# Kernel tuning notes

Measured on AMD Instinct MI355X. Metric: run time of the kernel, lower is better.

## Reference

```python
import jax, jax.numpy as jnp
import numpy as np

D = 128; H = 8; L = 3; FF = 512; HID = 512
B = 512; N = 20
KD = D // H
CLIP = 10.0


def _bn(x, g, b):
    # BatchNorm1d over flattened (B*n, D), training-mode batch stats, affine
    m = jnp.mean(x, axis=(0, 1)); v = jnp.var(x, axis=(0, 1))
    return (x - m) * jax.lax.rsqrt(v + 1e-5) * g + b


def _mha(x, Wq, Wk, Wv, Wo):
    q = jnp.einsum('bnd,hdk->hbnk', x, Wq)
    k = jnp.einsum('bnd,hdk->hbnk', x, Wk)
    v = jnp.einsum('bnd,hdk->hbnk', x, Wv)
    a = jax.nn.softmax(jnp.einsum('hbnk,hbmk->hbnm', q, k) / np.float32(np.sqrt(KD)), axis=-1)
    h = jnp.einsum('hbnm,hbmk->hbnk', a, v)
    return jnp.einsum('hbnk,hkd->bnd', h, Wo)


def _encode(x, Wq, Wk, Wv, Wo, g1, b1, fW1, fb1, fW2, fb2, g2, b2):
    for l in range(L):
        x = _bn(x + _mha(x, Wq[l], Wk[l], Wv[l], Wo[l]), g1[l], b1[l])
        f = jnp.maximum(x @ fW1[l] + fb1[l], 0.0) @ fW2[l] + fb2[l]
        x = _bn(x + f, g2[l], b2[l])
    return x


def _forward(coords, Wi, bi, W_ph, enc_Wq, enc_Wk, enc_Wv, enc_Wo, enc_g1, enc_b1,
             enc_ffW1, enc_ffb1, enc_ffW2, enc_ffb2, enc_g2, enc_b2,
             W_node, W_fixed, W_step, W_out, Wc1, bc1, Wc2, bc2):
    Bs, Ns, _ = coords.shape
    bid = jnp.arange(Bs)
    x = coords @ Wi + bi                                   # (B,N,D) initial embeddings
    crd = coords
    node_idx = jnp.broadcast_to(jnp.arange(Ns)[None, :], (Bs, Ns))
    # state is re-made each step, so step context is always the placeholder
    step_ctx = jnp.broadcast_to(W_ph[None, :], (Bs, 2 * D))
    ctx_q = step_ctx @ W_step                              # (B,D), constant across steps
    log_ps = []; irs = []; vals = []; tours = []
    first = prev = cur = None
    for i in range(Ns):  # sequential decode loop (shapes shrink each step)
        n = Ns - i
        E = _encode(x, enc_Wq, enc_Wk, enc_Wv, enc_Wo, enc_g1, enc_b1,
                    enc_ffW1, enc_ffb1, enc_ffW2, enc_ffb2, enc_g2, enc_b2)  # (B,n,D)
        g_mean = jnp.mean(E, axis=1)                       # (B,D)
        q = g_mean @ W_fixed + ctx_q                       # (B,D)
        gK, gV, lK = jnp.split(E @ W_node, 3, axis=-1)     # each (B,n,D)
        qh = q.reshape(Bs, H, KD)
        a = jax.nn.softmax(jnp.einsum('bhk,bnhk->bhn', qh, gK.reshape(Bs, n, H, KD)) / np.float32(np.sqrt(KD)), axis=-1)
        glimpse = jnp.einsum('bhn,bnhk->bhk', a, gV.reshape(Bs, n, H, KD)).reshape(Bs, D) @ W_out
        logits = jnp.tanh(jnp.einsum('bd,bnd->bn', glimpse, lK) / np.float32(np.sqrt(D))) * CLIP
        log_p = jax.nn.log_softmax(logits, axis=-1)        # mask all-False (fresh state)
        sel = jnp.argmax(log_p, axis=1)                    # greedy decode
        log_ps.append(log_p[bid, sel])
        cur = crd[bid, sel]
        if i == 0:
            first = cur
            irs.append(jnp.zeros((Bs,), coords.dtype))
        else:
            irs.append(-jnp.sqrt(jnp.sum((cur - prev) ** 2, axis=1)))
        h = jnp.maximum(jnp.concatenate([g_mean, step_ctx], axis=1) @ Wc1 + bc1, 0.0)
        vals.append((h @ Wc2 + bc2)[:, 0])
        tours.append(node_idx[bid, sel])
        if i < Ns - 1:
            sel_mask = (jnp.arange(n)[None, :] == sel[:, None]).astype(jnp.int32)
            keep = jnp.argsort(sel_mask, axis=1)[:, : n - 1]  # stable: drops selected, keeps order
            crd = jnp.take_along_axis(crd, keep[:, :, None], axis=1)
            x = jnp.take_along_axis(x, keep[:, :, None], axis=1)
            node_idx = jnp.take_along_axis(node_idx, keep, axis=1)
        prev = cur
    reward_final = -jnp.sqrt(jnp.sum((first - cur) ** 2, axis=1))
    tours = jnp.stack(tours, axis=1)                        # (B,N) int
    d = jnp.take_along_axis(coords, tours[:, :, None], axis=1)
    cost = jnp.sum(jnp.linalg.norm(d[:, 1:] - d[:, :-1], axis=2), axis=1) + jnp.linalg.norm(d[:, 0] - d[:, -1], axis=1)
    return (jnp.stack(log_ps, 1), jnp.stack(irs, 1), jnp.stack(vals, 1), cost, reward_final, tours)


def setup_inputs():
    key = jax.random.key(0)
    ks = jax.random.split(key, 16)
    def nrm(k, shp, scale=0.02):
        return jax.random.normal(k, shp, dtype=jnp.float32) * scale
    return {
        'coords': jax.random.uniform(ks[0], (B, N, 2), dtype=jnp.float32),
        'Wi': nrm(ks[1], (2, D), 0.5),
        'bi': jnp.zeros((D,), jnp.float32),
        'W_ph': jax.random.uniform(ks[2], (2 * D,), jnp.float32, -1.0, 1.0),
        'enc_Wq': nrm(ks[3], (L, H, D, KD)),
        'enc_Wk': nrm(ks[4], (L, H, D, KD)),
        'enc_Wv': nrm(ks[5], (L, H, D, KD)),
        'enc_Wo': nrm(ks[6], (L, H, KD, D)),
        'enc_g1': jnp.ones((L, D), jnp.float32),
        'enc_b1': jnp.zeros((L, D), jnp.float32),
        'enc_ffW1': nrm(ks[7], (L, D, FF)),
        'enc_ffb1': jnp.zeros((L, FF), jnp.float32),
        'enc_ffW2': nrm(ks[8], (L, FF, D)),
        'enc_ffb2': jnp.zeros((L, D), jnp.float32),
        'enc_g2': jnp.ones((L, D), jnp.float32),
        'enc_b2': jnp.zeros((L, D), jnp.float32),
        'W_node': nrm(ks[9], (D, 3 * D)),
        'W_fixed': nrm(ks[10], (D, D)),
        'W_step': nrm(ks[11], (2 * D, D)),
        'W_out': nrm(ks[12], (D, D)),
        'Wc1': nrm(ks[13], (3 * D, HID)),
        'bc1': jnp.zeros((HID,), jnp.float32),
        'Wc2': nrm(ks[14], (HID, 1)),
        'bc2': jnp.zeros((1,), jnp.float32),
    }


def reference(coords, Wi, bi, W_ph, enc_Wq, enc_Wk, enc_Wv, enc_Wo, enc_g1, enc_b1,
              enc_ffW1, enc_ffb1, enc_ffW2, enc_ffb2, enc_g2, enc_b2,
              W_node, W_fixed, W_step, W_out, Wc1, bc1, Wc2, bc2):
    return _forward(coords, Wi, bi, W_ph, enc_Wq, enc_Wk, enc_Wv, enc_Wo, enc_g1, enc_b1,
                    enc_ffW1, enc_ffb1, enc_ffW2, enc_ffb2, enc_g2, enc_b2,
                    W_node, W_fixed, W_step, W_out, Wc1, bc1, Wc2, bc2)
```

## Files before the change

### kernel.cpp

```cpp
#include <hip/hip_runtime.h>
#include <cmath>

namespace {
constexpr int Hc = 8, FFc = 512, HIDc = 512;
}

struct Params {
  const float *coords, *Wi, *bi, *W_ph;
  const float *Wq, *Wk, *Wv, *Wo, *g1, *b1, *fW1, *fb1, *fW2, *fb2, *g2, *b2;
  const float *W_node, *W_fixed, *W_step, *W_out, *Wc1, *bc1, *Wc2, *bc2;
  float* out;
};

__device__ __align__(16) float g_bn[120 * 8 * 256];
__device__ __align__(16) float g_x[512 * 2560];
__device__ __align__(16) float g_t[512 * 2560];
__device__ __align__(16) float g_h[512 * 2560];
__device__ __align__(16) float g_dec[512 * 7680];
__device__ __align__(16) float g_qv[512 * 128];
__device__ float g_val[512];
__device__ __align__(16) float g_crd[512 * 40];
__device__ int   g_idx[512 * 20];
__device__ float g_state[512 * 8];
__device__ __align__(16) float g_ctxq[128];
__device__ __align__(16) float g_cctx[512];
__device__ __align__(16) float g_Wqp[3 * 16384];
__device__ __align__(16) float g_Wkp[3 * 16384];
__device__ __align__(16) float g_Wvp[3 * 16384];
__device__ __align__(16) float g_Wop[3 * 16384];
__device__ __align__(16) float g_W1q[3 * 65536];
__device__ __align__(16) float g_W2q[3 * 65536];
__device__ __align__(16) float g_Wnp[49152];
__device__ __align__(16) float g_Wfp[16384];
__device__ __align__(16) float g_Woup[16384];
__device__ __align__(16) float g_Wc1p[65536];

#define DOT4(a, b) ((a).x*(b).x + (a).y*(b).y + (a).z*(b).z + (a).w*(b).w)

__device__ __forceinline__ void bn_coef(int slot, const float* g, const float* bb, float cnt,
                                        float* s_scale, float* s_shift, int tid) {
  if (tid < 128) {
    float sm = 0.f, sq = 0.f;
#pragma unroll
    for (int r = 0; r < 8; r++) {
      const float* s = &g_bn[(slot * 8 + r) * 256];
      sm += s[tid]; sq += s[128 + tid];
    }
    float m_ = sm / cnt;
    float v_ = sq / cnt - m_ * m_;
    float rs = rsqrtf(v_ + 1e-5f);
    float sc = rs * g[tid];
    s_scale[tid] = sc;
    s_shift[tid] = bb[tid] - m_ * sc;
  }
}

__global__ __launch_bounds__(256) void kinit(Params p) {
  const int tid = threadIdx.x, b = blockIdx.x;
  const int gid = b * 256 + tid, GS = 512 * 256;
  for (int i = gid; i < 120 * 8 * 256; i += GS) g_bn[i] = 0.f;
  if (gid < 512) g_val[gid] = 0.f;
  for (int e = tid; e < 2560; e += 256) {
    int i = e >> 7, d = e & 127;
    float cx = p.coords[b * 40 + 2 * i], cy = p.coords[b * 40 + 2 * i + 1];
    g_x[b * 2560 + e] = cx * p.Wi[d] + cy * p.Wi[128 + d] + p.bi[d];
  }
  if (tid < 40) g_crd[b * 40 + tid] = p.coords[b * 40 + tid];
  if (tid < 20) g_idx[b * 20 + tid] = tid;
  if (tid < 8) g_state[b * 8 + tid] = 0.f;
  if (b == 0) {
    if (tid < 128) {
      float a = 0.f;
      for (int j = 0; j < 256; j++) a += p.W_ph[j] * p.W_step[j * 128 + tid];
      g_ctxq[tid] = a;
    }
    for (int jj = tid; jj < 512; jj += 256) {
      float a = p.bc1[jj];
      for (int e = 0; e < 256; e++) a += p.W_ph[e] * p.Wc1[(128 + e) * 512 + jj];
      g_cctx[jj] = a;
    }
  }
  for (int e = gid; e < 3 * 16384; e += GS) {
    int sub = e & 3, rest = e >> 2;
    int j = rest & 127, rest2 = rest >> 7, d4 = rest2 & 31, l = rest2 >> 5;
    int d = d4 * 4 + sub;
    int src = l * 16384 + (j >> 4) * 2048 + d * 16 + (j & 15);
    g_Wqp[e] = p.Wq[src]; g_Wkp[e] = p.Wk[src]; g_Wvp[e] = p.Wv[src];
    int c = d;
    g_Wop[e] = p.Wo[l * 16384 + (c >> 4) * 2048 + (c & 15) * 128 + j];
  }
  for (int e = gid; e < 3 * 65536; e += GS) {
    int sub = e & 3, f = (e >> 2) & 16383, l = e >> 16;
    int cg = f & 127, c = (f >> 7) & 3, k4 = f >> 9;
    g_W1q[e] = p.fW1[l * 65536 + (k4 * 4 + sub) * 512 + cg * 4 + c];
  }
  for (int e = gid; e < 3 * 65536; e += GS) {
    int sub = e & 3, f = (e >> 2) & 16383, l = e >> 16;
    int j = f & 127, k4 = f >> 7;
    g_W2q[e] = p.fW2[l * 65536 + (k4 * 4 + sub) * 128 + j];
  }
  for (int e = gid; e < 49152; e += GS) {
    int sub = e & 3, rest = e >> 2;
    int col = rest % 384, e4 = rest / 384;
    g_Wnp[e] = p.W_node[(e4 * 4 + sub) * 384 + col];
  }
  for (int e = gid; e < 16384; e += GS) {
    int sub = e & 3, rest = e >> 2;
    int j = rest & 127, e4 = rest >> 7;
    g_Wfp[e] = p.W_fixed[(e4 * 4 + sub) * 128 + j];
    g_Woup[e] = p.W_out[(e4 * 4 + sub) * 128 + j];
  }
  for (int e = gid; e < 65536; e += GS) {
    int sub = e & 3, rest = e >> 2;
    int jj = rest & 511, e4 = rest >> 9;
    g_Wc1p[e] = p.Wc1[(e4 * 4 + sub) * 512 + jj];
  }
}

__global__ __launch_bounds__(256, 4) void ka1(Params p, int step, int l) {
  const int tid = threadIdx.x, b = blockIdx.x, hb = blockIdx.y;
  const int n = 20 - step;
  const int jc = tid & 63, rg = tid >> 6;
  __shared__ __align__(16) float s_t[2560];
  __shared__ __align__(16) float s_q[1280];
  __shared__ float s_kT[1280];
  __shared__ __align__(16) float s_v[1280];
  __shared__ float s_att[1600];
  __shared__ __align__(16) float s_scale[128], s_shift[128];

  if (l > 0)
    bn_coef(step * 6 + (l - 1) * 2 + 1, p.g2 + (l - 1) * 128, p.b2 + (l - 1) * 128,
            (float)(512 * n), s_scale, s_shift, tid);
  __syncthreads();
  const float4* src4 = (const float4*)((l == 0 ? g_x : g_t) + b * 2560);
  float4* st4 = (float4*)s_t;
  for (int e4 = tid; e4 < n * 32; e4 += 256) {
    float4 x = src4[e4];
    if (l > 0) {
      float4 sc = ((const float4*)s_scale)[e4 & 31];
      float4 sh = ((const float4*)s_shift)[e4 & 31];
      x.x = x.x * sc.x + sh.x; x.y = x.y * sc.y + sh.y;
      x.z = x.z * sc.z + sh.z; x.w = x.w * sc.w + sh.w;
    }
    st4[e4] = x;
  }
  __syncthreads();
  {
    const int j = hb * 64 + jc;
    const float4* wq4 = (const float4*)g_Wqp + l * 4096 + j;
    const float4* wk4 = (const float4*)g_Wkp + l * 4096 + j;
    const float4* wv4 = (const float4*)g_Wvp + l * 4096 + j;
    float aq[5], ak[5], av[5];
#pragma unroll
    for (int r = 0; r < 5; r++) { aq[r] = 0.f; ak[r] = 0.f; av[r] = 0.f; }
    float4 bq = wq4[0], bk = wk4[0], bv = wv4[0];
#pragma unroll 2
    for (int d4 = 0; d4 < 32; d4++) {
      const int dn = (d4 + 1) & 31;
      float4 nq = wq4[dn * 128], nk = wk4[dn * 128], nv = wv4[dn * 128];
#pragma unroll
      for (int r = 0; r < 5; r++) {
        int i = rg + 4 * r;
        if (i < n) {
          float4 x = st4[i * 32 + d4];
          aq[r] += DOT4(x, bq); ak[r] += DOT4(x, bk); av[r] += DOT4(x, bv);
        }
      }
      bq = nq; bk = nk; bv = nv;
    }
#pragma unroll
    for (int r = 0; r < 5; r++) {
      int i = rg + 4 * r;
      if (i < n) {
        s_q[i * 64 + jc] = aq[r];
        s_kT[jc * 20 + i] = ak[r];
        s_v[i * 64 + jc] = av[r];
      }
    }
  }
  __syncthreads();
  const int nn = n * n;
  for (int e = tid; e < 4 * nn; e += 256) {
    int hl = e / nn, rem = e % nn, i = rem / n, m = rem % n;
    float dacc = 0.f;
#pragma unroll
    for (int k2 = 0; k2 < 16; k2++)
      dacc += s_q[i * 64 + hl * 16 + k2] * s_kT[(hl * 16 + k2) * 20 + m];
    s_att[hl * 400 + i * 20 + m] = dacc * 0.25f;
  }
  __syncthreads();
  for (int r = tid; r < 4 * n; r += 256) {
    int hl = r / n, i = r % n;
    float* row = s_att + hl * 400 + i * 20;
    float mx = row[0];
    for (int m = 1; m < n; m++) mx = fmaxf(mx, row[m]);
    float s = 0.f;
    for (int m = 0; m < n; m++) { float ev = __expf(row[m] - mx); row[m] = ev; s += ev; }
    float inv = 1.f / s;
    for (int m = 0; m < n; m++) row[m] *= inv;
  }
  __syncthreads();
  for (int e = tid; e < 4 * n * 16; e += 256) {
    int hl = e / (n * 16), rem = e % (n * 16), i = rem >> 4, k2 = rem & 15;
    const float* arow = s_att + hl * 400 + i * 20;
    float acc = 0.f;
    for (int m = 0; m < n; m++) acc += arow[m] * s_v[m * 64 + hl * 16 + k2];
    g_h[b * 2560 + i * 128 + hb * 64 + hl * 16 + k2] = acc;
  }
}

__global__ __launch_bounds__(256, 4) void ka2(Params p, int step, int l) {
  const int tid = threadIdx.x, b = blockIdx.x, s = blockIdx.y;
  const int n = 20 - step;
  const int jcol = tid & 127, rhalf = tid >> 7;
  __shared__ __align__(16) float s_h[2560];
  __shared__ __align__(16) float s_x[2560];
  __shared__ __align__(16) float s_scale[128], s_shift[128];
  __shared__ float s_sm[128], s_sq[128];

  if (l > 0)
    bn_coef(step * 6 + (l - 1) * 2 + 1, p.g2 + (l - 1) * 128, p.b2 + (l - 1) * 128,
            (float)(512 * n), s_scale, s_shift, tid);
  __syncthreads();
  const float4* src4 = (const float4*)((l == 0 ? g_x : g_t) + b * 2560);
  const float4* gh4 = (const float4*)(g_h + b * 2560);
  float4* sh4 = (float4*)s_h;
  float4* sx4 = (float4*)s_x;
  for (int e4 = tid; e4 < n * 32; e4 += 256) {
    int i = e4 >> 5;
    if (((i ^ s) & 1) == 0) {
      sh4[e4] = gh4[e4];
      float4 x = src4[e4];
      if (l > 0) {
        float4 sc = ((const float4*)s_scale)[e4 & 31];
        float4 sf = ((const float4*)s_shift)[e4 & 31];
        x.x = x.x * sc.x + sf.x; x.y = x.y * sc.y + sf.y;
        x.z = x.z * sc.z + sf.z; x.w = x.w * sc.w + sf.w;
      }
      sx4[e4] = x;
    }
  }
  __syncthreads();
  float acc[5];
#pragma unroll
  for (int r = 0; r < 5; r++) {
    int i = s + 2 * (rhalf + 2 * r);
    acc[r] = (i < n) ? s_x[i * 128 + jcol] : 0.f;
  }
  const float4* wo4 = (const float4*)g_Wop + l * 4096 + jcol;
  float4 wb0 = wo4[0], wb1 = wo4[128];
#pragma unroll 2
  for (int c4 = 0; c4 < 32; c4++) {
    float4 wn = wo4[((c4 + 2) & 31) * 128];
#pragma unroll
    for (int r = 0; r < 5; r++) {
      int i = s + 2 * (rhalf + 2 * r);
      if (i < n) { float4 h = sh4[i * 32 + c4]; acc[r] += DOT4(h, wb0); }
    }
    wb0 = wb1; wb1 = wn;
  }
  float sm = 0.f, sq = 0.f;
#pragma unroll
  for (int r = 0; r < 5; r++) {
    int i = s + 2 * (rhalf + 2 * r);
    if (i < n) { g_t[b * 2560 + i * 128 + jcol] = acc[r]; sm += acc[r]; sq += acc[r] * acc[r]; }
  }
  __syncthreads();
  if (rhalf == 1) { s_sm[jcol] = sm; s_sq[jcol] = sq; }
  __syncthreads();
  if (rhalf == 0) {
    float* slot = &g_bn[((step * 6 + l * 2) * 8 + ((b * 2 + s) & 7)) * 256];
    atomicAdd(&slot[jcol], sm + s_sm[jcol]);
    atomicAdd(&slot[128 + jcol], sq + s_sq[jcol]);
  }
}

__global__ __launch_bounds__(256, 4) void kff(Params p, int step, int l) {
  const int tid = threadIdx.x, bx = blockIdx.x;
  const int n = 20 - step;
  const int r0 = bx * 16;
  const int wid = tid >> 6, lam = tid & 63;
  const int g = wid >> 1, rh = wid & 1;
  __shared__ __align__(16) float s_x[16 * 128];
  __shared__ __align__(16) float s_hid[16 * 512];
  __shared__ __align__(16) float s_scale[128], s_shift[128];
  __shared__ float s_bn[8 * 128 * 2];

  bn_coef(step * 6 + l * 2, p.g1 + l * 128, p.b1 + l * 128, (float)(512 * n), s_scale, s_shift, tid);
  __syncthreads();
  {
    float4* sx4 = (float4*)s_x;
    for (int e4 = tid; e4 < 16 * 32; e4 += 256) {
      int row = e4 >> 5, d4 = e4 & 31;
      int r = r0 + row, b = r / n, i = r - b * n;
      float4 x = *(const float4*)(g_t + b * 2560 + i * 128 + d4 * 4);
      float4 sc = ((const float4*)s_scale)[d4];
      float4 sf = ((const float4*)s_shift)[d4];
      x.x = x.x * sc.x + sf.x; x.y = x.y * sc.y + sf.y;
      x.z = x.z * sc.z + sf.z; x.w = x.w * sc.w + sf.w;
      sx4[e4] = x;
    }
  }
  __syncthreads();
  {
    const int cg = g * 64 + lam;
    float acc[8][4];
#pragma unroll
    for (int rr = 0; rr < 8; rr++)
#pragma unroll
      for (int c = 0; c < 4; c++) acc[rr][c] = 0.f;
    const float4* w1 = (const float4*)g_W1q + l * 16384 + cg;
    const float4* xx = (const float4*)s_x + rh * 8 * 32;
    float4 wb[4];
#pragma unroll
    for (int c = 0; c < 4; c++) wb[c] = w1[c * 128];
#pragma unroll 2
    for (int k4 = 0; k4 < 32; k4++) {
      float4 wn[4];
      const int kn = (k4 + 1) & 31;
#pragma unroll
      for (int c = 0; c < 4; c++) wn[c] = w1[kn * 512 + c * 128];
#pragma unroll
      for (int rr = 0; rr < 8; rr++) {
        float4 xr = xx[rr * 32 + k4];
#pragma unroll
        for (int c = 0; c < 4; c++) acc[rr][c] += DOT4(xr, wb[c]);
      }
#pragma unroll
      for (int c = 0; c < 4; c++) wb[c] = wn[c];
    }
    float4 b1v = *(const float4*)(p.fb1 + l * FFc + cg * 4);
#pragma unroll
    for (int rr = 0; rr < 8; rr++) {
      int row = rh * 8 + rr;
      float4 u;
      u.x = fmaxf(acc[rr][0] + b1v.x, 0.f); u.y = fmaxf(acc[rr][1] + b1v.y, 0.f);
      u.z = fmaxf(acc[rr][2] + b1v.z, 0.f); u.w = fmaxf(acc[rr][3] + b1v.w, 0.f);
      *(float4*)&s_hid[row * 512 + cg * 4] = u;
    }
  }
  __syncthreads();
  {
    const int j = g * 64 + lam;
    float acc[8];
#pragma unroll
    for (int rr = 0; rr < 8; rr++) acc[rr] = 0.f;
    const float4* w2 = (const float4*)g_W2q + l * 16384 + j;
    const float4* hh = (const float4*)s_hid + rh * 8 * 128;
    float4 wb0 = w2[0], wb1 = w2[128];
#pragma unroll 2
    for (int k4 = 0; k4 < 128; k4++) {
      float4 wn = w2[((k4 + 2) & 127) * 128];
#pragma unroll
      for (int rr = 0; rr < 8; rr++) acc[rr] += DOT4(hh[rr * 128 + k4], wb0);
      wb0 = wb1; wb1 = wn;
    }
    const float f2 = p.fb2[l * 128 + j];
    float u[8];
#pragma unroll
    for (int rr = 0; rr < 8; rr++) {
      int row = rh * 8 + rr;
      int r = r0 + row, b = r / n, i = r - b * n;
      u[rr] = s_x[row * 128 + j] + acc[rr] + f2;
      g_t[b * 2560 + i * 128 + j] = u[rr];
    }
#pragma unroll
    for (int q = 0; q < 4; q++) {
      const int sb = ((rh * 4 + q) * 128 + j) * 2;
      s_bn[sb] = u[2 * q] + u[2 * q + 1];
      s_bn[sb + 1] = u[2 * q] * u[2 * q] + u[2 * q + 1] * u[2 * q + 1];
    }
  }
  __syncthreads();
  if (tid < 128) {
    float sm = 0.f, sq = 0.f;
#pragma unroll
    for (int rg = 0; rg < 8; rg++) { sm += s_bn[(rg * 128 + tid) * 2]; sq += s_bn[(rg * 128 + tid) * 2 + 1]; }
    float* slot = &g_bn[((step * 6 + l * 2 + 1) * 8 + (bx & 7)) * 256];
    atomicAdd(&slot[tid], sm);
    atomicAdd(&slot[128 + tid], sq);
  }
}

__global__ __launch_bounds__(256, 4) void kd1(Params p, int step) {
  const int tid = threadIdx.x, b = blockIdx.x, bc = blockIdx.y;
  const int n = 20 - step;
  const int cb = tid & 63, rg = tid >> 6;
  __shared__ __align__(16) float s_t[2560];
  __shared__ __align__(16) float s_scale[128], s_shift[128];
  __shared__ __align__(16) float s_gmean[128];
  __shared__ float s_red[256];

  bn_coef(step * 6 + 5, p.g2 + 2 * 128, p.b2 + 2 * 128, (float)(512 * n), s_scale, s_shift, tid);
  __syncthreads();
  const float4* src4 = (const float4*)(g_t + b * 2560);
  float4* st4 = (float4*)s_t;
  for (int e4 = tid; e4 < n * 32; e4 += 256) {
    float4 x = src4[e4];
    float4 sc = ((const float4*)s_scale)[e4 & 31];
    float4 sf = ((const float4*)s_shift)[e4 & 31];
    x.x = x.x * sc.x + sf.x; x.y = x.y * sc.y + sf.y;
    x.z = x.z * sc.z + sf.z; x.w = x.w * sc.w + sf.w;
    st4[e4] = x;
  }
  __syncthreads();
  if (tid < 128) {
    float ssum = 0.f;
    for (int i2 = 0; i2 < n; i2++) ssum += s_t[i2 * 128 + tid];
    s_gmean[tid] = ssum / (float)n;
  }
  __syncthreads();
  {
    float acc[3][5];
#pragma unroll
    for (int cc = 0; cc < 3; cc++)
#pragma unroll
      for (int r = 0; r < 5; r++) acc[cc][r] = 0.f;
    const float4* wn4 = (const float4*)g_Wnp + bc * 192 + cb;
    float4 b0 = wn4[0], b1 = wn4[64], b2 = wn4[128];
#pragma unroll 2
    for (int d4 = 0; d4 < 32; d4++) {
      const int dn = (d4 + 1) & 31;
      float4 n0 = wn4[dn * 384], n1 = wn4[dn * 384 + 64], n2 = wn4[dn * 384 + 128];
#pragma unroll
      for (int r = 0; r < 5; r++) {
        int i = rg + 4 * r;
        if (i < n) {
          float4 x = st4[i * 32 + d4];
          acc[0][r] += DOT4(x, b0); acc[1][r] += DOT4(x, b1); acc[2][r] += DOT4(x, b2);
        }
      }
      b0 = n0; b1 = n1; b2 = n2;
    }
#pragma unroll
    for (int r = 0; r < 5; r++) {
      int i = rg + 4 * r;
      if (i < n) {
#pragma unroll
        for (int cc = 0; cc < 3; cc++)
          g_dec[b * 7680 + i * 384 + bc * 192 + cb + 64 * cc] = acc[cc][r];
      }
    }
  }
  {
    int jj = bc * 256 + tid;
    float a = g_cctx[jj];
    const float4* wc4 = (const float4*)g_Wc1p + jj;
    const float4* gm4 = (const float4*)s_gmean;
    float4 wb0 = wc4[0], wb1 = wc4[512];
#pragma unroll 2
    for (int e4 = 0; e4 < 32; e4++) {
      float4 wn = wc4[((e4 + 2) & 31) * 512];
      float4 g = gm4[e4]; a += DOT4(g, wb0);
      wb0 = wb1; wb1 = wn;
    }
    s_red[tid] = fmaxf(a, 0.f) * p.Wc2[jj];
  }
  __syncthreads();
#pragma unroll
  for (int sred = 128; sred > 0; sred >>= 1) {
    if (tid < sred) s_red[tid] += s_red[tid + sred];
    __syncthreads();
  }
  if (tid == 0) atomicAdd(&g_val[b], s_red[0]);
  if (bc == 0 && tid < 128) {
    float a = g_ctxq[tid];
    const float4* wf4 = (const float4*)g_Wfp + tid;
    const float4* gm4 = (const float4*)s_gmean;
    float4 wb0 = wf4[0], wb1 = wf4[128];
#pragma unroll 2
    for (int e4 = 0; e4 < 32; e4++) {
      float4 wn = wf4[((e4 + 2) & 31) * 128];
      float4 g = gm4[e4]; a += DOT4(g, wb0);
      wb0 = wb1; wb1 = wn;
    }
    g_qv[b * 128 + tid] = a;
  }
}

__global__ __launch_bounds__(256) void kd2(Params p, int step) {
  const int tid = threadIdx.x, b = blockIdx.x;
  const int n = 20 - step;
  __shared__ __align__(16) float s_dec[7680];
  __shared__ float s_qv[128], s_glq[128];
  __shared__ __align__(16) float s_red[128];
  __shared__ float s_att[160];
  __shared__ float s_logits[20];
  __shared__ int s_sel;

  {
    const float4* src4 = (const float4*)(g_dec + b * 7680);
    float4* sd4 = (float4*)s_dec;
    for (int e4 = tid; e4 < n * 96; e4 += 256) sd4[e4] = src4[e4];
    if (tid < 128) s_qv[tid] = g_qv[b * 128 + tid];
  }
  __syncthreads();
  for (int e = tid; e < Hc * n; e += 256) {
    int hh = e / n, m = e % n;
    float dacc = 0.f;
#pragma unroll
    for (int k2 = 0; k2 < 16; k2++) dacc += s_qv[hh * 16 + k2] * s_dec[m * 384 + hh * 16 + k2];
    s_att[hh * 20 + m] = dacc * 0.25f;
  }
  __syncthreads();
  if (tid < Hc) {
    float* row = s_att + tid * 20;
    float mx = row[0];
    for (int m = 1; m < n; m++) mx = fmaxf(mx, row[m]);
    float s = 0.f;
    for (int m = 0; m < n; m++) { float ev = __expf(row[m] - mx); row[m] = ev; s += ev; }
    float inv = 1.f / s;
    for (int m = 0; m < n; m++) row[m] *= inv;
  }
  __syncthreads();
  if (tid < 128) {
    int hh = tid >> 4;
    const float* arow = s_att + hh * 20;
    float acc = 0.f;
    for (int m = 0; m < n; m++) acc += arow[m] * s_dec[m * 384 + 128 + tid];
    s_red[tid] = acc;
  }
  __syncthreads();
  if (tid < 128) {
    float a = 0.f;
    const float4* wo4 = (const float4*)g_Woup + tid;
    const float4* rr4 = (const float4*)s_red;
    float4 wb0 = wo4[0], wb1 = wo4[128];
#pragma unroll 2
    for (int c4 = 0; c4 < 32; c4++) {
      float4 wn = wo4[((c4 + 2) & 31) * 128];
      float4 r = rr4[c4]; a += DOT4(r, wb0);
      wb0 = wb1; wb1 = wn;
    }
    s_glq[tid] = a;
  }
  __syncthreads();
  if (tid < n) {
    const float* lk = s_dec + tid * 384 + 256;
    float dacc = 0.f;
    for (int d = 0; d < 128; d++) dacc += s_glq[d] * lk[d];
    s_logits[tid] = 10.f * tanhf(dacc / 11.313708498984761f);
  }
  __syncthreads();
  if (tid == 0) {
    float mx = s_logits[0]; int sel = 0;
    for (int i2 = 1; i2 < n; i2++) if (s_logits[i2] > mx) { mx = s_logits[i2]; sel = i2; }
    float s = 0.f;
    for (int i2 = 0; i2 < n; i2++) s += __expf(s_logits[i2] - mx);
    p.out[b * 20 + step] = -logf(s);
    float cx = g_crd[b * 40 + 2 * sel], cy = g_crd[b * 40 + 2 * sel + 1];
    float ir = 0.f;
    if (step > 0) {
      float dx = cx - g_state[b * 8 + 0], dy = cy - g_state[b * 8 + 1];
      float dist = sqrtf(dx * dx + dy * dy);
      ir = -dist;
      g_state[b * 8 + 4] += dist;
    } else { g_state[b * 8 + 2] = cx; g_state[b * 8 + 3] = cy; g_state[b * 8 + 4] = 0.f; }
    p.out[10240 + b * 20 + step] = ir;
    p.out[31744 + b * 20 + step] = (float)g_idx[b * 20 + sel];
    g_state[b * 8 + 0] = cx; g_state[b * 8 + 1] = cy;
    if (step == 19) {
      float dx = g_state[b * 8 + 2] - cx, dy = g_state[b * 8 + 3] - cy;
      float dc = sqrtf(dx * dx + dy * dy);
      p.out[31232 + b] = -dc;
      p.out[30720 + b] = g_state[b * 8 + 4] + dc;
    }
    p.out[20480 + b * 20 + step] = g_val[b] + p.bc2[0];
    g_val[b] = 0.f;
    s_sel = sel;
  }
  __syncthreads();
  if (step < 19) {
    const int sel = s_sel;
    const int movecnt = (n - 1 - sel) * 128;
    float tmp[10]; float crdv = 0.f; int idxv = 0;
#pragma unroll
    for (int r = 0; r < 10; r++) { int e = tid + r * 256; if (e < movecnt) tmp[r] = g_x[b * 2560 + (sel + 1) * 128 + e]; }
    const int mc2 = (n - 1 - sel) * 2;
    if (tid < mc2) crdv = g_crd[b * 40 + (sel + 1) * 2 + tid];
    if (tid < n - 1 - sel) idxv = g_idx[b * 20 + sel + 1 + tid];
    __syncthreads();
#pragma unroll
    for (int r = 0; r < 10; r++) { int e = tid + r * 256; if (e < movecnt) g_x[b * 2560 + sel * 128 + e] = tmp[r]; }
    if (tid < mc2) g_crd[b * 40 + sel * 2 + tid] = crdv;
    if (tid < n - 1 - sel) g_idx[b * 20 + sel + tid] = idxv;
  }
}

extern "C" void kernel_launch(void* const* d_in, const int* in_sizes, int n_in,
                              void* d_out, int out_size, void* d_ws, size_t ws_size,
                              hipStream_t stream) {
  Params p;
  p.coords  = (const float*)d_in[0];
  p.Wi      = (const float*)d_in[1];
  p.bi      = (const float*)d_in[2];
  p.W_ph    = (const float*)d_in[3];
  p.Wq      = (const float*)d_in[4];
  p.Wk      = (const float*)d_in[5];
  p.Wv      = (const float*)d_in[6];
  p.Wo      = (const float*)d_in[7];
  p.g1      = (const float*)d_in[8];
  p.b1      = (const float*)d_in[9];
  p.fW1     = (const float*)d_in[10];
  p.fb1     = (const float*)d_in[11];
  p.fW2     = (const float*)d_in[12];
  p.fb2     = (const float*)d_in[13];
  p.g2      = (const float*)d_in[14];
  p.b2      = (const float*)d_in[15];
  p.W_node  = (const float*)d_in[16];
  p.W_fixed = (const float*)d_in[17];
  p.W_step  = (const float*)d_in[18];
  p.W_out   = (const float*)d_in[19];
  p.Wc1     = (const float*)d_in[20];
  p.bc1     = (const float*)d_in[21];
  p.Wc2     = (const float*)d_in[22];
  p.bc2     = (const float*)d_in[23];
  p.out = (float*)d_out;

  kinit<<<512, 256, 0, stream>>>(p);
  for (int step = 0; step < 20; step++) {
    const int n = 20 - step;
    for (int l = 0; l < 3; l++) {
      ka1<<<dim3(512, 2), 256, 0, stream>>>(p, step, l);
      ka2<<<dim3(512, 2), 256, 0, stream>>>(p, step, l);
      kff<<<dim3(32 * n), 256, 0, stream>>>(p, step, l);
    }
    kd1<<<dim3(512, 2), 256, 0, stream>>>(p, step);
    kd2<<<512, 256, 0, stream>>>(p, step);
  }
}
```

Baseline: 6.258 ms.

## Fuse attention halves and decoder kernels into single 512-thread blocks

```diff
diff --git a/kernel.cpp b/kernel.cpp
--- a/kernel.cpp
+++ b/kernel.cpp
@@ -15,10 +15,6 @@
 __device__ __align__(16) float g_bn[120 * 8 * 256];
 __device__ __align__(16) float g_x[512 * 2560];
 __device__ __align__(16) float g_t[512 * 2560];
-__device__ __align__(16) float g_h[512 * 2560];
-__device__ __align__(16) float g_dec[512 * 7680];
-__device__ __align__(16) float g_qv[512 * 128];
-__device__ float g_val[512];
 __device__ __align__(16) float g_crd[512 * 40];
 __device__ int   g_idx[512 * 20];
 __device__ float g_state[512 * 8];
@@ -59,7 +55,6 @@
   const int tid = threadIdx.x, b = blockIdx.x;
   const int gid = b * 256 + tid, GS = 512 * 256;
   for (int i = gid; i < 120 * 8 * 256; i += GS) g_bn[i] = 0.f;
-  if (gid < 512) g_val[gid] = 0.f;
   for (int e = tid; e < 2560; e += 256) {
     int i = e >> 7, d = e & 127;
     float cx = p.coords[b * 40 + 2 * i], cy = p.coords[b * 40 + 2 * i + 1];
@@ -117,16 +112,16 @@
   }
 }
 
-__global__ __launch_bounds__(256, 4) void ka1(Params p, int step, int l) {
-  const int tid = threadIdx.x, b = blockIdx.x, hb = blockIdx.y;
+__global__ __launch_bounds__(512, 4) void ka(Params p, int step, int l) {
+  const int tid = threadIdx.x, b = blockIdx.x;
   const int n = 20 - step;
-  const int jc = tid & 63, rg = tid >> 6;
   __shared__ __align__(16) float s_t[2560];
-  __shared__ __align__(16) float s_q[1280];
-  __shared__ float s_kT[1280];
-  __shared__ __align__(16) float s_v[1280];
-  __shared__ float s_att[1600];
+  __shared__ __align__(16) float s_q[2560];
+  __shared__ float s_kT[2560];
+  __shared__ __align__(16) float s_v[2560];
+  __shared__ float s_att[3200];
   __shared__ __align__(16) float s_scale[128], s_shift[128];
+  __shared__ float s_bnp[4 * 128 * 2];
 
   if (l > 0)
     bn_coef(step * 6 + (l - 1) * 2 + 1, p.g2 + (l - 1) * 128, p.b2 + (l - 1) * 128,
@@ -134,7 +129,7 @@
   __syncthreads();
   const float4* src4 = (const float4*)((l == 0 ? g_x : g_t) + b * 2560);
   float4* st4 = (float4*)s_t;
-  for (int e4 = tid; e4 < n * 32; e4 += 256) {
+  for (int e4 = tid; e4 < n * 32; e4 += 512) {
     float4 x = src4[e4];
     if (l > 0) {
       float4 sc = ((const float4*)s_scale)[e4 & 31];
@@ -146,7 +141,7 @@
   }
   __syncthreads();
   {
-    const int j = hb * 64 + jc;
+    const int j = tid & 127, rg2 = tid >> 7;
     const float4* wq4 = (const float4*)g_Wqp + l * 4096 + j;
     const float4* wk4 = (const float4*)g_Wkp + l * 4096 + j;
     const float4* wv4 = (const float4*)g_Wvp + l * 4096 + j;
@@ -160,7 +155,7 @@
       float4 nq = wq4[dn * 128], nk = wk4[dn * 128], nv = wv4[dn * 128];
 #pragma unroll
       for (int r = 0; r < 5; r++) {
-        int i = rg + 4 * r;
+        int i = rg2 + 4 * r;
         if (i < n) {
           float4 x = st4[i * 32 + d4];
           aq[r] += DOT4(x, bq); ak[r] += DOT4(x, bk); av[r] += DOT4(x, bv);
@@ -170,26 +165,26 @@
     }
 #pragma unroll
     for (int r = 0; r < 5; r++) {
-      int i = rg + 4 * r;
+      int i = rg2 + 4 * r;
       if (i < n) {
-        s_q[i * 64 + jc] = aq[r];
-        s_kT[jc * 20 + i] = ak[r];
-        s_v[i * 64 + jc] = av[r];
+        s_q[i * 128 + j] = aq[r];
+        s_kT[j * 20 + i] = ak[r];
+        s_v[i * 128 + j] = av[r];
       }
     }
   }
   __syncthreads();
   const int nn = n * n;
-  for (int e = tid; e < 4 * nn; e += 256) {
+  for (int e = tid; e < 8 * nn; e += 512) {
     int hl = e / nn, rem = e % nn, i = rem / n, m = rem % n;
     float dacc = 0.f;
 #pragma unroll
     for (int k2 = 0; k2 < 16; k2++)
-      dacc += s_q[i * 64 + hl * 16 + k2] * s_kT[(hl * 16 + k2) * 20 + m];
+      dacc += s_q[i * 128 + hl * 16 + k2] * s_kT[(hl * 16 + k2) * 20 + m];
     s_att[hl * 400 + i * 20 + m] = dacc * 0.25f;
   }
   __syncthreads();
-  for (int r = tid; r < 4 * n; r += 256) {
+  for (int r = tid; r < 8 * n; r += 512) {
     int hl = r / n, i = r % n;
     float* row = s_att + hl * 400 + i * 20;
     float mx = row[0];
@@ -200,78 +195,53 @@
     for (int m = 0; m < n; m++) row[m] *= inv;
   }
   __syncthreads();
-  for (int e = tid; e < 4 * n * 16; e += 256) {
+  for (int e = tid; e < 8 * n * 16; e += 512) {
     int hl = e / (n * 16), rem = e % (n * 16), i = rem >> 4, k2 = rem & 15;
     const float* arow = s_att + hl * 400 + i * 20;
     float acc = 0.f;
-    for (int m = 0; m < n; m++) acc += arow[m] * s_v[m * 64 + hl * 16 + k2];
-    g_h[b * 2560 + i * 128 + hb * 64 + hl * 16 + k2] = acc;
-  }
-}
-
-__global__ __launch_bounds__(256, 4) void ka2(Params p, int step, int l) {
-  const int tid = threadIdx.x, b = blockIdx.x, s = blockIdx.y;
-  const int n = 20 - step;
-  const int jcol = tid & 127, rhalf = tid >> 7;
-  __shared__ __align__(16) float s_h[2560];
-  __shared__ __align__(16) float s_x[2560];
-  __shared__ __align__(16) float s_scale[128], s_shift[128];
-  __shared__ float s_sm[128], s_sq[128];
-
-  if (l > 0)
-    bn_coef(step * 6 + (l - 1) * 2 + 1, p.g2 + (l - 1) * 128, p.b2 + (l - 1) * 128,
-            (float)(512 * n), s_scale, s_shift, tid);
-  __syncthreads();
-  const float4* src4 = (const float4*)((l == 0 ? g_x : g_t) + b * 2560);
-  const float4* gh4 = (const float4*)(g_h + b * 2560);
-  float4* sh4 = (float4*)s_h;
-  float4* sx4 = (float4*)s_x;
-  for (int e4 = tid; e4 < n * 32; e4 += 256) {
-    int i = e4 >> 5;
-    if (((i ^ s) & 1) == 0) {
-      sh4[e4] = gh4[e4];
-      float4 x = src4[e4];
-      if (l > 0) {
-        float4 sc = ((const float4*)s_scale)[e4 & 31];
-        float4 sf = ((const float4*)s_shift)[e4 & 31];
-        x.x = x.x * sc.x + sf.x; x.y = x.y * sc.y + sf.y;
-        x.z = x.z * sc.z + sf.z; x.w = x.w * sc.w + sf.w;
-      }
-      sx4[e4] = x;
-    }
-  }
-  __syncthreads();
-  float acc[5];
-#pragma unroll
-  for (int r = 0; r < 5; r++) {
-    int i = s + 2 * (rhalf + 2 * r);
-    acc[r] = (i < n) ? s_x[i * 128 + jcol] : 0.f;
-  }
-  const float4* wo4 = (const float4*)g_Wop + l * 4096 + jcol;
-  float4 wb0 = wo4[0], wb1 = wo4[128];
-#pragma unroll 2
-  for (int c4 = 0; c4 < 32; c4++) {
-    float4 wn = wo4[((c4 + 2) & 31) * 128];
+    for (int m = 0; m < n; m++) acc += arow[m] * s_v[m * 128 + hl * 16 + k2];
+    s_q[i * 128 + hl * 16 + k2] = acc;
+  }
+  __syncthreads();
+  {
+    const int j2 = tid & 127, rh2 = tid >> 7;
+    const int s = rh2 & 1, rhalf = rh2 >> 1;
+    const float4* sh4 = (const float4*)s_q;
+    float acc[5];
 #pragma unroll
     for (int r = 0; r < 5; r++) {
       int i = s + 2 * (rhalf + 2 * r);
-      if (i < n) { float4 h = sh4[i * 32 + c4]; acc[r] += DOT4(h, wb0); }
-    }
-    wb0 = wb1; wb1 = wn;
-  }
-  float sm = 0.f, sq = 0.f;
-#pragma unroll
-  for (int r = 0; r < 5; r++) {
-    int i = s + 2 * (rhalf + 2 * r);
-    if (i < n) { g_t[b * 2560 + i * 128 + jcol] = acc[r]; sm += acc[r]; sq += acc[r] * acc[r]; }
-  }
-  __syncthreads();
-  if (rhalf == 1) { s_sm[jcol] = sm; s_sq[jcol] = sq; }
-  __syncthreads();
-  if (rhalf == 0) {
-    float* slot = &g_bn[((step * 6 + l * 2) * 8 + ((b * 2 + s) & 7)) * 256];
-    atomicAdd(&slot[jcol], sm + s_sm[jcol]);
-    atomicAdd(&slot[128 + jcol], sq + s_sq[jcol]);
+      acc[r] = (i < n) ? s_t[i * 128 + j2] : 0.f;
+    }
+    const float4* wo4 = (const float4*)g_Wop + l * 4096 + j2;
+    float4 wb0 = wo4[0], wb1 = wo4[128];
+#pragma unroll 2
+    for (int c4 = 0; c4 < 32; c4++) {
+      float4 wn = wo4[((c4 + 2) & 31) * 128];
+#pragma unroll
+      for (int r = 0; r < 5; r++) {
+        int i = s + 2 * (rhalf + 2 * r);
+        if (i < n) { float4 h = sh4[i * 32 + c4]; acc[r] += DOT4(h, wb0); }
+      }
+      wb0 = wb1; wb1 = wn;
+    }
+    float sm = 0.f, sq = 0.f;
+#pragma unroll
+    for (int r = 0; r < 5; r++) {
+      int i = s + 2 * (rhalf + 2 * r);
+      if (i < n) { g_t[b * 2560 + i * 128 + j2] = acc[r]; sm += acc[r]; sq += acc[r] * acc[r]; }
+    }
+    s_bnp[(rh2 * 128 + j2) * 2] = sm;
+    s_bnp[(rh2 * 128 + j2) * 2 + 1] = sq;
+  }
+  __syncthreads();
+  if (tid < 128) {
+    float sm = 0.f, sq = 0.f;
+#pragma unroll
+    for (int h = 0; h < 4; h++) { sm += s_bnp[(h * 128 + tid) * 2]; sq += s_bnp[(h * 128 + tid) * 2 + 1]; }
+    float* slot = &g_bn[((step * 6 + l * 2) * 8 + (b & 7)) * 256];
+    atomicAdd(&slot[tid], sm);
+    atomicAdd(&slot[128 + tid], sq);
   }
 }
 
@@ -382,20 +352,25 @@
   }
 }
 
-__global__ __launch_bounds__(256, 4) void kd1(Params p, int step) {
-  const int tid = threadIdx.x, b = blockIdx.x, bc = blockIdx.y;
+__global__ __launch_bounds__(512, 4) void kd(Params p, int step) {
+  const int tid = threadIdx.x, b = blockIdx.x;
   const int n = 20 - step;
-  const int cb = tid & 63, rg = tid >> 6;
   __shared__ __align__(16) float s_t[2560];
+  __shared__ __align__(16) float s_dec[7680];
   __shared__ __align__(16) float s_scale[128], s_shift[128];
   __shared__ __align__(16) float s_gmean[128];
-  __shared__ float s_red[256];
+  __shared__ float s_red[512];
+  __shared__ float s_qv[128], s_glq[128];
+  __shared__ __align__(16) float s_gl[128];
+  __shared__ float s_att[160];
+  __shared__ float s_logits[20];
+  __shared__ int s_sel;
 
   bn_coef(step * 6 + 5, p.g2 + 2 * 128, p.b2 + 2 * 128, (float)(512 * n), s_scale, s_shift, tid);
   __syncthreads();
   const float4* src4 = (const float4*)(g_t + b * 2560);
   float4* st4 = (float4*)s_t;
-  for (int e4 = tid; e4 < n * 32; e4 += 256) {
+  for (int e4 = tid; e4 < n * 32; e4 += 512) {
     float4 x = src4[e4];
     float4 sc = ((const float4*)s_scale)[e4 & 31];
     float4 sf = ((const float4*)s_shift)[e4 & 31];
@@ -411,39 +386,46 @@
   }
   __syncthreads();
   {
-    float acc[3][5];
-#pragma unroll
-    for (int cc = 0; cc < 3; cc++)
-#pragma unroll
-      for (int r = 0; r < 5; r++) acc[cc][r] = 0.f;
-    const float4* wn4 = (const float4*)g_Wnp + bc * 192 + cb;
-    float4 b0 = wn4[0], b1 = wn4[64], b2 = wn4[128];
+    const int cb = tid & 63, rg = tid >> 6;
+    float acc[6][3];
+#pragma unroll
+    for (int cc = 0; cc < 6; cc++)
+#pragma unroll
+      for (int r = 0; r < 3; r++) acc[cc][r] = 0.f;
+    const float4* wn4 = (const float4*)g_Wnp + cb;
+    float4 wb[6];
+#pragma unroll
+    for (int cc = 0; cc < 6; cc++) wb[cc] = wn4[cc * 64];
 #pragma unroll 2
     for (int d4 = 0; d4 < 32; d4++) {
       const int dn = (d4 + 1) & 31;
-      float4 n0 = wn4[dn * 384], n1 = wn4[dn * 384 + 64], n2 = wn4[dn * 384 + 128];
-#pragma unroll
-      for (int r = 0; r < 5; r++) {
-        int i = rg + 4 * r;
+      float4 wn[6];
+#pragma unroll
+      for (int cc = 0; cc < 6; cc++) wn[cc] = wn4[dn * 384 + cc * 64];
+#pragma unroll
+      for (int r = 0; r < 3; r++) {
+        int i = rg + 8 * r;
         if (i < n) {
           float4 x = st4[i * 32 + d4];
-          acc[0][r] += DOT4(x, b0); acc[1][r] += DOT4(x, b1); acc[2][r] += DOT4(x, b2);
+#pragma unroll
+          for (int cc = 0; cc < 6; cc++) acc[cc][r] += DOT4(x, wb[cc]);
         }
       }
-      b0 = n0; b1 = n1; b2 = n2;
-    }
-#pragma unroll
-    for (int r = 0; r < 5; r++) {
-      int i = rg + 4 * r;
+#pragma unroll
+      for (int cc = 0; cc < 6; cc++) wb[cc] = wn[cc];
+    }
+#pragma unroll
+    for (int r = 0; r < 3; r++) {
+      int i = rg + 8 * r;
       if (i < n) {
 #pragma unroll
-        for (int cc = 0; cc < 3; cc++)
-          g_dec[b * 7680 + i * 384 + bc * 192 + cb + 64 * cc] = acc[cc][r];
+        for (int cc = 0; cc < 6; cc++)
+          s_dec[i * 384 + cb + 64 * cc] = acc[cc][r];
       }
     }
   }
   {
-    int jj = bc * 256 + tid;
+    const int jj = tid;
     float a = g_cctx[jj];
     const float4* wc4 = (const float4*)g_Wc1p + jj;
     const float4* gm4 = (const float4*)s_gmean;
@@ -456,14 +438,7 @@
     }
     s_red[tid] = fmaxf(a, 0.f) * p.Wc2[jj];
   }
-  __syncthreads();
-#pragma unroll
-  for (int sred = 128; sred > 0; sred >>= 1) {
-    if (tid < sred) s_red[tid] += s_red[tid + sred];
-    __syncthreads();
-  }
-  if (tid == 0) atomicAdd(&g_val[b], s_red[0]);
-  if (bc == 0 && tid < 128) {
+  if (tid < 128) {
     float a = g_ctxq[tid];
     const float4* wf4 = (const float4*)g_Wfp + tid;
     const float4* gm4 = (const float4*)s_gmean;
@@ -474,28 +449,15 @@
       float4 g = gm4[e4]; a += DOT4(g, wb0);
       wb0 = wb1; wb1 = wn;
     }
-    g_qv[b * 128 + tid] = a;
-  }
-}
-
-__global__ __launch_bounds__(256) void kd2(Params p, int step) {
-  const int tid = threadIdx.x, b = blockIdx.x;
-  const int n = 20 - step;
-  __shared__ __align__(16) float s_dec[7680];
-  __shared__ float s_qv[128], s_glq[128];
-  __shared__ __align__(16) float s_red[128];
-  __shared__ float s_att[160];
-  __shared__ float s_logits[20];
-  __shared__ int s_sel;
-
-  {
-    const float4* src4 = (const float4*)(g_dec + b * 7680);
-    float4* sd4 = (float4*)s_dec;
-    for (int e4 = tid; e4 < n * 96; e4 += 256) sd4[e4] = src4[e4];
-    if (tid < 128) s_qv[tid] = g_qv[b * 128 + tid];
-  }
-  __syncthreads();
-  for (int e = tid; e < Hc * n; e += 256) {
+    s_qv[tid] = a;
+  }
+  __syncthreads();
+#pragma unroll
+  for (int sred = 256; sred > 0; sred >>= 1) {
+    if (tid < sred) s_red[tid] += s_red[tid + sred];
+    __syncthreads();
+  }
+  for (int e = tid; e < Hc * n; e += 512) {
     int hh = e / n, m = e % n;
     float dacc = 0.f;
 #pragma unroll
@@ -518,13 +480,13 @@
     const float* arow = s_att + hh * 20;
     float acc = 0.f;
     for (int m = 0; m < n; m++) acc += arow[m] * s_dec[m * 384 + 128 + tid];
-    s_red[tid] = acc;
+    s_gl[tid] = acc;
   }
   __syncthreads();
   if (tid < 128) {
     float a = 0.f;
     const float4* wo4 = (const float4*)g_Woup + tid;
-    const float4* rr4 = (const float4*)s_red;
+    const float4* rr4 = (const float4*)s_gl;
     float4 wb0 = wo4[0], wb1 = wo4[128];
 #pragma unroll 2
     for (int c4 = 0; c4 < 32; c4++) {
@@ -565,23 +527,22 @@
       p.out[31232 + b] = -dc;
       p.out[30720 + b] = g_state[b * 8 + 4] + dc;
     }
-    p.out[20480 + b * 20 + step] = g_val[b] + p.bc2[0];
-    g_val[b] = 0.f;
+    p.out[20480 + b * 20 + step] = s_red[0] + p.bc2[0];
     s_sel = sel;
   }
   __syncthreads();
   if (step < 19) {
     const int sel = s_sel;
     const int movecnt = (n - 1 - sel) * 128;
-    float tmp[10]; float crdv = 0.f; int idxv = 0;
-#pragma unroll
-    for (int r = 0; r < 10; r++) { int e = tid + r * 256; if (e < movecnt) tmp[r] = g_x[b * 2560 + (sel + 1) * 128 + e]; }
+    float tmp[5]; float crdv = 0.f; int idxv = 0;
+#pragma unroll
+    for (int r = 0; r < 5; r++) { int e = tid + r * 512; if (e < movecnt) tmp[r] = g_x[b * 2560 + (sel + 1) * 128 + e]; }
     const int mc2 = (n - 1 - sel) * 2;
     if (tid < mc2) crdv = g_crd[b * 40 + (sel + 1) * 2 + tid];
     if (tid < n - 1 - sel) idxv = g_idx[b * 20 + sel + 1 + tid];
     __syncthreads();
 #pragma unroll
-    for (int r = 0; r < 10; r++) { int e = tid + r * 256; if (e < movecnt) g_x[b * 2560 + sel * 128 + e] = tmp[r]; }
+    for (int r = 0; r < 5; r++) { int e = tid + r * 512; if (e < movecnt) g_x[b * 2560 + sel * 128 + e] = tmp[r]; }
     if (tid < mc2) g_crd[b * 40 + sel * 2 + tid] = crdv;
     if (tid < n - 1 - sel) g_idx[b * 20 + sel + tid] = idxv;
   }
@@ -621,11 +582,9 @@
   for (int step = 0; step < 20; step++) {
     const int n = 20 - step;
     for (int l = 0; l < 3; l++) {
-      ka1<<<dim3(512, 2), 256, 0, stream>>>(p, step, l);
-      ka2<<<dim3(512, 2), 256, 0, stream>>>(p, step, l);
+      ka<<<512, 512, 0, stream>>>(p, step, l);
       kff<<<dim3(32 * n), 256, 0, stream>>>(p, step, l);
     }
-    kd1<<<dim3(512, 2), 256, 0, stream>>>(p, step);
-    kd2<<<512, 256, 0, stream>>>(p, step);
-  }
-}
+    kd<<<512, 512, 0, stream>>>(p, step);
+  }
+}
```

After: 5.679 ms (median of 2 runs). 9.3% less time.
